# Optimization experiments

Measured on AMD Instinct MI355X. Metric: run time of the kernel, lower is better.

The kernel has to match this reference:

```python
import jax, jax.numpy as jnp
import numpy as np

N_V, N_E, NNZ = 200000, 40000, 1000000
D_IN, D_V, D_E = 128, 128, 128


def setup_inputs() -> dict:
    key = jax.random.key(0)
    ks = jax.random.split(key, 16)
    inp = {
        "vfeat": jax.random.normal(ks[0], (N_V, D_IN), jnp.float32),
        "efeat": jax.random.normal(ks[1], (N_E, D_E), jnp.float32),
        "v_reg_weight": jax.random.uniform(ks[2], (N_V, 1), jnp.float32, 0.1, 1.0),
        "v_reg_sum": jax.random.uniform(ks[3], (N_V, 1), jnp.float32, 0.5, 2.0),
        "e_reg_weight": jax.random.uniform(ks[4], (N_E, 1), jnp.float32, 0.1, 1.0),
        "e_reg_sum": jax.random.uniform(ks[5], (N_E, 1), jnp.float32, 0.5, 2.0),
        "node_idx": jax.random.randint(ks[6], (NNZ,), 0, N_V, jnp.int32),
        "edge_idx": jax.random.randint(ks[7], (NNZ,), 0, N_E, jnp.int32),
        "W1": jax.random.normal(ks[8], (D_IN, D_V), jnp.float32) / np.sqrt(D_IN),
        "b1": jnp.zeros((D_V,), jnp.float32),
        "Wve": jax.random.normal(ks[9], (D_V, D_E), jnp.float32) / np.sqrt(D_V),
        "bve": jnp.zeros((D_E,), jnp.float32),
        "Wev": jax.random.normal(ks[10], (D_E, D_V), jnp.float32) / np.sqrt(D_E),
        "bev": jnp.zeros((D_V,), jnp.float32),
        "first_layer": 1,
        "last_layer": 1,
    }
    return inp


def reference(vfeat, efeat, v_reg_weight, v_reg_sum, e_reg_weight, e_reg_sum,
              node_idx, edge_idx, W1, b1, Wve, bve, Wev, bev,
              first_layer, last_layer):
    # vertex projection (first_layer selects which Linear; math identical shape-wise)
    feat_v = vfeat @ W1 + b1                       # [N_V, D_V]
    # --- 'in' etype: vertex -> hyperedge weighted aggregation ---
    Wh_v = feat_v @ Wve + bve                      # [N_V, D_E]
    w_in = v_reg_weight[node_idx] / e_reg_sum[edge_idx]           # [NNZ, 1]
    msg_in = w_in * Wh_v[node_idx]                 # [NNZ, D_E]
    feat_e = jax.ops.segment_sum(msg_in, edge_idx, num_segments=N_E)
    # --- 'con' etype: hyperedge -> vertex weighted aggregation ---
    Wh_e = feat_e @ Wev + bev                      # [N_E, D_V]
    w_con = e_reg_weight[edge_idx] / v_reg_sum[node_idx]          # [NNZ, 1]
    msg_con = w_con * Wh_e[edge_idx]               # [NNZ, D_V]
    feat_v_out = jax.ops.segment_sum(msg_con, node_idx, num_segments=N_V)
    return feat_v_out, feat_e
```

## Files before the change

kernel.cpp:

```cpp
#include <hip/hip_runtime.h>


#define BM 128
#define BK 32

static __device__ __forceinline__ float4 f4add(float4 a, float4 b) {
    return make_float4(a.x + b.x, a.y + b.y, a.z + b.z, a.w + b.w);
}

__global__ void fuse_weights(const float* __restrict__ W1, const float* __restrict__ b1,
                             const float* __restrict__ Wve, const float* __restrict__ bve,
                             float* __restrict__ Wf, float* __restrict__ bf) {
    int i = blockIdx.x;
    int j = threadIdx.x;
    float acc = 0.f;
    if (i < 128) {
        #pragma unroll 8
        for (int k = 0; k < 128; ++k)
            acc = fmaf(W1[i * 128 + k], Wve[k * 128 + j], acc);
        Wf[i * 128 + j] = acc;
    } else {
        #pragma unroll 8
        for (int k = 0; k < 128; ++k)
            acc = fmaf(b1[k], Wve[k * 128 + j], acc);
        bf[j] = acc + bve[j];
    }
}

__global__ __launch_bounds__(256)
void gemm128(const float* __restrict__ A, const float* __restrict__ B,
             const float* __restrict__ bias, const float* __restrict__ rowscale,
             float* __restrict__ out, int M) {
    __shared__ float As[BK][BM];
    __shared__ float Bs[BK][128];

    const int t = threadIdx.x;
    const int row0 = blockIdx.x * BM;
    const int tx = t & 15;
    const int ty = t >> 4;
    const int m0 = ty * 8;
    const int n0 = tx * 8;

    float acc[8][8];
    #pragma unroll
    for (int i = 0; i < 8; ++i)
        #pragma unroll
        for (int j = 0; j < 8; ++j) acc[i][j] = 0.f;

    for (int k0 = 0; k0 < 128; k0 += BK) {
        #pragma unroll
        for (int p = 0; p < 4; ++p) {
            int f = t + p * 256;
            int r = f >> 3;
            int cv = f & 7;
            int gr = row0 + r;
            float4 v = make_float4(0.f, 0.f, 0.f, 0.f);
            if (gr < M) v = *(const float4*)(&A[(size_t)gr * 128 + k0 + cv * 4]);
            As[cv * 4 + 0][r] = v.x;
            As[cv * 4 + 1][r] = v.y;
            As[cv * 4 + 2][r] = v.z;
            As[cv * 4 + 3][r] = v.w;
        }
        #pragma unroll
        for (int p = 0; p < 4; ++p) {
            int f = t + p * 256;
            int r = f >> 5;
            int cv = f & 31;
            *(float4*)(&Bs[r][cv * 4]) = *(const float4*)(&B[(size_t)(k0 + r) * 128 + cv * 4]);
        }
        __syncthreads();

        #pragma unroll
        for (int k = 0; k < BK; ++k) {
            float a[8], b[8];
            *(float4*)&a[0] = *(const float4*)&As[k][m0];
            *(float4*)&a[4] = *(const float4*)&As[k][m0 + 4];
            *(float4*)&b[0] = *(const float4*)&Bs[k][n0];
            *(float4*)&b[4] = *(const float4*)&Bs[k][n0 + 4];
            #pragma unroll
            for (int i = 0; i < 8; ++i)
                #pragma unroll
                for (int j = 0; j < 8; ++j)
                    acc[i][j] = fmaf(a[i], b[j], acc[i][j]);
        }
        __syncthreads();
    }

    float bb[8];
    #pragma unroll
    for (int j = 0; j < 8; ++j) bb[j] = bias[n0 + j];

    #pragma unroll
    for (int i = 0; i < 8; ++i) {
        int gr = row0 + m0 + i;
        if (gr < M) {
            float rs = rowscale[gr];
            float o[8];
            #pragma unroll
            for (int j = 0; j < 8; ++j) o[j] = (acc[i][j] + bb[j]) * rs;
            *(float4*)(&out[(size_t)gr * 128 + n0]) = *(float4*)&o[0];
            *(float4*)(&out[(size_t)gr * 128 + n0 + 4]) = *(float4*)&o[4];
        }
    }
}

__global__ __launch_bounds__(256)
void hist(const int* __restrict__ node_idx, const int* __restrict__ edge_idx,
          int* __restrict__ cnt_e, int* __restrict__ cnt_v, int nnz) {
    int i = blockIdx.x * 256 + threadIdx.x;
    if (i < nnz) {
        atomicAdd(&cnt_e[edge_idx[i]], 1);
        atomicAdd(&cnt_v[node_idx[i]], 1);
    }
}

__global__ __launch_bounds__(256)
void alloc_ranges(const int* __restrict__ cnt_e, const int* __restrict__ cnt_v,
                  int* __restrict__ start_e, int* __restrict__ cursor_e,
                  int* __restrict__ start_v, int* __restrict__ cursor_v,
                  int* __restrict__ ctr, int ne, int nv) {
    int gid = blockIdx.x * 256 + threadIdx.x;
    int lane = threadIdx.x & 63;
    int total = ne + nv;
    if (gid - lane >= total) return;
    bool isE = gid < ne;
    int idx = isE ? gid : gid - ne;
    int c = (gid < total) ? (isE ? cnt_e[idx] : cnt_v[idx]) : 0;
    int x = c;
    #pragma unroll
    for (int d = 1; d < 64; d <<= 1) {
        int y = __shfl_up(x, d);
        if (lane >= d) x += y;
    }
    int base;
    if (lane == 63) base = atomicAdd(isE ? &ctr[0] : &ctr[1], x);
    base = __shfl(base, 63);
    int pos = base + (x - c);
    if (gid < total) {
        if (isE) { start_e[idx] = pos; cursor_e[idx] = pos; }
        else     { start_v[idx] = pos; cursor_v[idx] = pos; }
    }
}

__global__ __launch_bounds__(256)
void scatter(const int* __restrict__ node_idx, const int* __restrict__ edge_idx,
             int* __restrict__ cursor_e, int* __restrict__ cursor_v,
             int* __restrict__ src_e, int* __restrict__ src_v, int nnz) {
    int i = blockIdx.x * 256 + threadIdx.x;
    if (i < nnz) {
        int n = node_idx[i], e = edge_idx[i];
        int pe = atomicAdd(&cursor_e[e], 1);
        src_e[pe] = n;
        int pv = atomicAdd(&cursor_v[n], 1);
        src_v[pv] = e;
    }
}

__global__ __launch_bounds__(256)
void gather_rows(const float* __restrict__ src, const int* __restrict__ srcidx,
                 const int* __restrict__ start, const int* __restrict__ cnt,
                 const float* __restrict__ sum_tbl, float* __restrict__ dst, int nseg) {
    const int lane = threadIdx.x & 31;
    int seg = (blockIdx.x * 256 + threadIdx.x) >> 5;
    if (seg >= nseg) return;
    const int st = start[seg];
    const int len = cnt[seg];
    const int c4 = lane * 4;
    float4 a0 = make_float4(0, 0, 0, 0), a1 = a0, a2 = a0, a3 = a0;
    int j = 0;
    for (; j + 4 <= len; j += 4) {
        int n0 = srcidx[st + j + 0];
        int n1 = srcidx[st + j + 1];
        int n2 = srcidx[st + j + 2];
        int n3 = srcidx[st + j + 3];
        a0 = f4add(a0, *(const float4*)(&src[(size_t)n0 * 128 + c4]));
        a1 = f4add(a1, *(const float4*)(&src[(size_t)n1 * 128 + c4]));
        a2 = f4add(a2, *(const float4*)(&src[(size_t)n2 * 128 + c4]));
        a3 = f4add(a3, *(const float4*)(&src[(size_t)n3 * 128 + c4]));
    }
    for (; j < len; ++j) {
        int n = srcidx[st + j];
        a0 = f4add(a0, *(const float4*)(&src[(size_t)n * 128 + c4]));
    }
    float sc = 1.0f / sum_tbl[seg];
    float4 r = f4add(f4add(a0, a1), f4add(a2, a3));
    r.x *= sc; r.y *= sc; r.z *= sc; r.w *= sc;
    *(float4*)(&dst[(size_t)seg * 128 + c4]) = r;
}

extern "C" void kernel_launch(void* const* d_in, const int* in_sizes, int n_in,
                              void* d_out, int out_size, void* d_ws, size_t ws_size,
                              hipStream_t stream) {
    const float* vfeat        = (const float*)d_in[0];
    const float* v_reg_weight = (const float*)d_in[2];
    const float* v_reg_sum    = (const float*)d_in[3];
    const float* e_reg_weight = (const float*)d_in[4];
    const float* e_reg_sum    = (const float*)d_in[5];
    const int*   node_idx     = (const int*)d_in[6];
    const int*   edge_idx     = (const int*)d_in[7];
    const float* W1           = (const float*)d_in[8];
    const float* b1           = (const float*)d_in[9];
    const float* Wve          = (const float*)d_in[10];
    const float* bve          = (const float*)d_in[11];
    const float* Wev          = (const float*)d_in[12];
    const float* bev          = (const float*)d_in[13];

    const int N_V = in_sizes[2];
    const int N_E = in_sizes[4];
    const int NNZ = in_sizes[6];

    char* w = (char*)d_ws;
    float* Wf       = (float*)(w + 0);
    float* bf       = (float*)(w + 65536);
    float* Whe      = (float*)(w + 66048);
    int*   cnt_e    = (int*)(w + 20546048);
    int*   cnt_v    = (int*)(w + 20706048);
    int*   ctr      = (int*)(w + 21506048);
    int*   start_e  = (int*)(w + 21506056);
    int*   cursor_e = (int*)(w + 21666056);
    int*   start_v  = (int*)(w + 21826056);
    int*   cursor_v = (int*)(w + 22626056);
    int*   src_e    = (int*)(w + 23426056);
    int*   src_v    = (int*)(w + 27426056);

    float* feat_v_out = (float*)d_out;
    float* feat_e     = (float*)d_out + (size_t)N_V * 128;
    float* Whv        = feat_v_out;

    hipMemsetAsync(w + 20546048, 0, 960008, stream);

    fuse_weights<<<129, 128, 0, stream>>>(W1, b1, Wve, bve, Wf, bf);

    hist<<<(NNZ + 255) / 256, 256, 0, stream>>>(node_idx, edge_idx, cnt_e, cnt_v, NNZ);

    alloc_ranges<<<(N_E + N_V + 255) / 256, 256, 0, stream>>>(
        cnt_e, cnt_v, start_e, cursor_e, start_v, cursor_v, ctr, N_E, N_V);

    gemm128<<<(N_V + BM - 1) / BM, 256, 0, stream>>>(vfeat, Wf, bf, v_reg_weight, Whv, N_V);

    scatter<<<(NNZ + 255) / 256, 256, 0, stream>>>(node_idx, edge_idx,
                                                   cursor_e, cursor_v, src_e, src_v, NNZ);

    gather_rows<<<(N_E * 32 + 255) / 256, 256, 0, stream>>>(
        Whv, src_e, start_e, cnt_e, e_reg_sum, feat_e, N_E);

    gemm128<<<(N_E + BM - 1) / BM, 256, 0, stream>>>(feat_e, Wev, bev, e_reg_weight, Whe, N_E);

    gather_rows<<<(N_V * 32 + 255) / 256, 256, 0, stream>>>(
        Whe, src_v, start_v, cnt_v, v_reg_sum, feat_v_out, N_V);
}
```

Before: 767.4 us.

## Partition histogram and scatter atomics by key range across block groups

The histogram and CSR scatter kernels now split blocks into 16 groups, 8 for edges and 8 for vertices, and each group handles only keys in one eighth of the segment range. Each group scans the whole index array with a grid-stride loop and does atomics only for keys in its range. The aim is to keep each group's atomic targets in a smaller address window for better L2 locality and less contention. The cost is that every index is read 8 times per key type, and the kernel runs a fixed 4096 blocks.

```diff
diff --git a/kernel.cpp b/kernel.cpp
--- a/kernel.cpp
+++ b/kernel.cpp
@@ -105,12 +105,23 @@
 }
 
 __global__ __launch_bounds__(256)
-void hist(const int* __restrict__ node_idx, const int* __restrict__ edge_idx,
-          int* __restrict__ cnt_e, int* __restrict__ cnt_v, int nnz) {
-    int i = blockIdx.x * 256 + threadIdx.x;
-    if (i < nnz) {
-        atomicAdd(&cnt_e[edge_idx[i]], 1);
-        atomicAdd(&cnt_v[node_idx[i]], 1);
+void hist16(const int* __restrict__ edge_idx, const int* __restrict__ node_idx,
+            int* __restrict__ cnt_e, int* __restrict__ cnt_v,
+            int nnz, int ne, int nv) {
+    const int g = blockIdx.x & 15;
+    const bool isE = g < 8;
+    const int sub = g & 7;
+    const int* key = isE ? edge_idx : node_idx;
+    int* cnt = isE ? cnt_e : cnt_v;
+    const int nseg = isE ? ne : nv;
+    const int lo = (int)((long long)nseg * sub / 8);
+    const int hi = (int)((long long)nseg * (sub + 1) / 8);
+    const int nb = gridDim.x >> 4;
+    const int bid = blockIdx.x >> 4;
+    const int stride = nb * 256;
+    for (int i = bid * 256 + threadIdx.x; i < nnz; i += stride) {
+        int k = key[i];
+        if (k >= lo && k < hi) atomicAdd(&cnt[k], 1);
     }
 }
 
@@ -143,16 +154,29 @@
 }
 
 __global__ __launch_bounds__(256)
-void scatter(const int* __restrict__ node_idx, const int* __restrict__ edge_idx,
-             int* __restrict__ cursor_e, int* __restrict__ cursor_v,
-             int* __restrict__ src_e, int* __restrict__ src_v, int nnz) {
-    int i = blockIdx.x * 256 + threadIdx.x;
-    if (i < nnz) {
-        int n = node_idx[i], e = edge_idx[i];
-        int pe = atomicAdd(&cursor_e[e], 1);
-        src_e[pe] = n;
-        int pv = atomicAdd(&cursor_v[n], 1);
-        src_v[pv] = e;
+void scatter16(const int* __restrict__ edge_idx, const int* __restrict__ node_idx,
+               int* __restrict__ cursor_e, int* __restrict__ cursor_v,
+               int* __restrict__ src_e, int* __restrict__ src_v,
+               int nnz, int ne, int nv) {
+    const int g = blockIdx.x & 15;
+    const bool isE = g < 8;
+    const int sub = g & 7;
+    const int* key = isE ? edge_idx : node_idx;
+    const int* pay = isE ? node_idx : edge_idx;
+    int* cursor = isE ? cursor_e : cursor_v;
+    int* out = isE ? src_e : src_v;
+    const int nseg = isE ? ne : nv;
+    const int lo = (int)((long long)nseg * sub / 8);
+    const int hi = (int)((long long)nseg * (sub + 1) / 8);
+    const int nb = gridDim.x >> 4;
+    const int bid = blockIdx.x >> 4;
+    const int stride = nb * 256;
+    for (int i = bid * 256 + threadIdx.x; i < nnz; i += stride) {
+        int k = key[i];
+        if (k >= lo && k < hi) {
+            int p = atomicAdd(&cursor[k], 1);
+            out[p] = pay[i];
+        }
     }
 }
 
@@ -231,15 +255,15 @@
 
     fuse_weights<<<129, 128, 0, stream>>>(W1, b1, Wve, bve, Wf, bf);
 
-    hist<<<(NNZ + 255) / 256, 256, 0, stream>>>(node_idx, edge_idx, cnt_e, cnt_v, NNZ);
+    hist16<<<4096, 256, 0, stream>>>(edge_idx, node_idx, cnt_e, cnt_v, NNZ, N_E, N_V);
 
     alloc_ranges<<<(N_E + N_V + 255) / 256, 256, 0, stream>>>(
         cnt_e, cnt_v, start_e, cursor_e, start_v, cursor_v, ctr, N_E, N_V);
 
     gemm128<<<(N_V + BM - 1) / BM, 256, 0, stream>>>(vfeat, Wf, bf, v_reg_weight, Whv, N_V);
 
-    scatter<<<(NNZ + 255) / 256, 256, 0, stream>>>(node_idx, edge_idx,
-                                                   cursor_e, cursor_v, src_e, src_v, NNZ);
+    scatter16<<<4096, 256, 0, stream>>>(edge_idx, node_idx,
+                                        cursor_e, cursor_v, src_e, src_v, NNZ, N_E, N_V);
 
     gather_rows<<<(N_E * 32 + 255) / 256, 256, 0, stream>>>(
         Whv, src_e, start_e, cnt_e, e_reg_sum, feat_e, N_E);
```

Result: faster. 683.7 us (-10.9%).
